# Performance work log

Measured on AMD Instinct MI355X. Metric: run time of the kernel, lower is better.

The kernel has to match this reference:

```python
import jax, jax.numpy as jnp
import numpy as np

B, S, D, H = 2, 2048, 1024, 16
DK = D // H  # 64


def setup_inputs() -> dict:
    key = jax.random.key(0)
    ks = jax.random.split(key, 12)
    inp = {
        "query": jax.random.normal(ks[0], (B, S, D), jnp.float32),
        "key": jax.random.normal(ks[1], (B, S, D), jnp.float32),
        "value": jax.random.normal(ks[2], (B, S, D), jnp.float32),
        "mask": jnp.ones((B, 1, S, S), jnp.float32),  # 1.0 = attend
    }
    sc = 1.0 / np.sqrt(D)
    inp["wq"] = jax.random.normal(ks[3], (D, D), jnp.float32) * sc
    inp["bq"] = jax.random.normal(ks[4], (D,), jnp.float32) * 0.01
    inp["wk"] = jax.random.normal(ks[5], (D, D), jnp.float32) * sc
    inp["bk"] = jax.random.normal(ks[6], (D,), jnp.float32) * 0.01
    inp["wv"] = jax.random.normal(ks[7], (D, D), jnp.float32) * sc
    inp["bv"] = jax.random.normal(ks[8], (D,), jnp.float32) * 0.01
    inp["wo"] = jax.random.normal(ks[9], (D, D), jnp.float32) * sc
    inp["bo"] = jax.random.normal(ks[10], (D,), jnp.float32) * 0.01
    return inp


def _split_heads(x):
    # [B, S, D] -> [B, H, S, DK]
    b, s, _ = x.shape
    return x.reshape(b, s, H, DK).transpose(0, 2, 1, 3)


def reference(query, key, value, mask, wq, bq, wk, bk, wv, bv, wo, bo):
    # Linear projections (torch Linear: x @ W.T + b)
    q = _split_heads(query @ wq.T + bq)   # [B,H,Sq,DK]
    k = _split_heads(key @ wk.T + bk)     # [B,H,Sk,DK]
    v = _split_heads(value @ wv.T + bv)   # [B,H,Sk,DK]

    attn = jnp.einsum('bhqd,bhkd->bhqk', q, k) / jnp.sqrt(jnp.float32(DK))
    # mask: 1.0 attend, 0.0 masked -> add finfo.min at masked positions
    inv = (1.0 - mask) * jnp.finfo(attn.dtype).min
    attn = attn + inv
    attention_weights = jax.nn.softmax(attn, axis=-1)  # [B,H,Sq,Sk]
    # dropout=0.0 (eval mode): identity
    ctx = jnp.einsum('bhqk,bhkd->bhqd', attention_weights, v)  # [B,H,Sq,DK]
    concat = ctx.transpose(0, 2, 1, 3).reshape(ctx.shape[0], ctx.shape[2], D)
    output = concat @ wo.T + bo
    return (output, attention_weights)
```

## Files before the change

kernel.cpp:

```cpp
#include <hip/hip_runtime.h>
#include <cstdint>

typedef short bf16x8 __attribute__((ext_vector_type(8)));
typedef float f32x4 __attribute__((ext_vector_type(4)));

#define NEG_MAX 3.402823466e38f

__device__ __forceinline__ unsigned short f2bf(float f) {
  uint32_t u = __builtin_bit_cast(uint32_t, f);
  u += 0x7FFFu + ((u >> 16) & 1u);
  return (unsigned short)(u >> 16);
}

__device__ __forceinline__ bf16x8 pack8(float4 x, float4 y) {
  bf16x8 r;
  r[0] = (short)f2bf(x.x); r[1] = (short)f2bf(x.y); r[2] = (short)f2bf(x.z); r[3] = (short)f2bf(x.w);
  r[4] = (short)f2bf(y.x); r[5] = (short)f2bf(y.y); r[6] = (short)f2bf(y.z); r[7] = (short)f2bf(y.w);
  return r;
}

__global__ __launch_bounds__(256) void cvt_w(const float* __restrict__ wq, const float* __restrict__ wk,
                                             const float* __restrict__ wv, const float* __restrict__ wo,
                                             unsigned short* __restrict__ out) {
  int i = blockIdx.x * 256 + threadIdx.x;
  const int sel = i >> 18;
  const int idx = i & 0x3FFFF;
  const float* src = (sel == 0) ? wq : (sel == 1) ? wk : (sel == 2) ? wv : wo;
  float4 v = reinterpret_cast<const float4*>(src)[idx];
  ushort4 o;
  o.x = f2bf(v.x); o.y = f2bf(v.y); o.z = f2bf(v.z); o.w = f2bf(v.w);
  reinterpret_cast<ushort4*>(out)[i] = o;
}

__global__ __launch_bounds__(256) void mask_scan(const float* __restrict__ mask,
                                                 int* __restrict__ flags) {
  const int blk = blockIdx.x;
  const int kt = blk & 31, qt = (blk >> 5) & 31, b = blk >> 10;
  const float* base = mask + ((size_t)b * 2048 + qt * 64) * 2048 + kt * 64;
  const int t = threadIdx.x;
  const int row = t >> 2, c0 = (t & 3) * 16;
  const float4* p = reinterpret_cast<const float4*>(base + (size_t)row * 2048 + c0);
  bool ones = true;
#pragma unroll
  for (int i = 0; i < 4; ++i) {
    float4 v = p[i];
    ones = ones && (v.x == 1.f) && (v.y == 1.f) && (v.z == 1.f) && (v.w == 1.f);
  }
  unsigned long long ball = __ballot(ones);
  __shared__ int sf[4];
  if ((t & 63) == 0) sf[t >> 6] = (ball == ~0ull) ? 1 : 0;
  __syncthreads();
  if (t == 0) flags[blk] = sf[0] & sf[1] & sf[2] & sf[3];
}

__global__ __launch_bounds__(256) void gemm_qkv(const float* __restrict__ Aq,
                                                const float* __restrict__ Ak,
                                                const float* __restrict__ Av,
                                                const unsigned short* __restrict__ W3,
                                                const float* __restrict__ bq,
                                                const float* __restrict__ bk,
                                                const float* __restrict__ bv,
                                                unsigned short* __restrict__ Qbf,
                                                unsigned short* __restrict__ Kbf,
                                                unsigned short* __restrict__ Vtb) {
  constexpr int KD = 1024;
  __shared__ __align__(16) unsigned short Al[128 * 32];
  __shared__ __align__(16) unsigned short Bl[128 * 32];
  const int tid = threadIdx.x;
  const int l = tid & 63;
  const int w = tid >> 6;
  const int lr = l & 15;
  const int lg = l >> 4;
  const int gm = blockIdx.y;
  const int gn = blockIdx.x;
  const int z = blockIdx.z;
  const int wr = w >> 1;
  const int wc = w & 1;

  const float* Af = (z == 0) ? Aq : (z == 1) ? Ak : Av;
  const float* bias = (z == 0) ? bq : (z == 1) ? bk : bv;
  const unsigned short* Bw = W3 + (size_t)z * 1048576;
  unsigned short* Cb = (z == 0) ? Qbf : (z == 1) ? Kbf : Vtb;

  f32x4 acc[4][4];
#pragma unroll
  for (int m = 0; m < 4; ++m)
#pragma unroll
    for (int n = 0; n < 4; ++n) acc[m][n] = (f32x4){0.f, 0.f, 0.f, 0.f};

  const int c0 = w * 2;
  const int srow = (l >> 2);
  const int scol = (l & 3) * 8;
  const unsigned short* gB = Bw + (size_t)(gn * 128) * KD;

  const int arow = tid >> 1;
  const int ahalf = tid & 1;
  const float* gA = Af + (size_t)(gm * 128 + arow) * KD + ahalf * 16;

  float4 ap[4];
  {
    const float4* p = reinterpret_cast<const float4*>(gA);
#pragma unroll
    for (int i = 0; i < 4; ++i) ap[i] = p[i];
  }

  for (int kt = 0; kt < 32; ++kt) {
    const int k0 = kt * 32;
    const unsigned short* b0 = gB + (size_t)(c0 * 16 + srow) * KD + k0 + scol;
    const unsigned short* b1 = b0 + (size_t)16 * KD;
    __builtin_amdgcn_global_load_lds((const __attribute__((address_space(1))) void*)b0,
                                     (__attribute__((address_space(3))) void*)&Bl[c0 * 512], 16, 0, 0);
    __builtin_amdgcn_global_load_lds((const __attribute__((address_space(1))) void*)b1,
                                     (__attribute__((address_space(3))) void*)&Bl[c0 * 512 + 512], 16, 0, 0);
    {
      bf16x8* dst = reinterpret_cast<bf16x8*>(&Al[arow * 32 + ahalf * 16]);
      dst[0] = pack8(ap[0], ap[1]);
      dst[1] = pack8(ap[2], ap[3]);
    }
    __syncthreads();
    if (kt + 1 < 32) {
      const float4* p = reinterpret_cast<const float4*>(gA + (kt + 1) * 32);
#pragma unroll
      for (int i = 0; i < 4; ++i) ap[i] = p[i];
    }
    bf16x8 af[4], bfr[4];
#pragma unroll
    for (int m = 0; m < 4; ++m)
      af[m] = *reinterpret_cast<const bf16x8*>(&Al[(wr * 64 + m * 16 + lr) * 32 + lg * 8]);
#pragma unroll
    for (int n = 0; n < 4; ++n)
      bfr[n] = *reinterpret_cast<const bf16x8*>(&Bl[(wc * 64 + n * 16 + lr) * 32 + lg * 8]);
#pragma unroll
    for (int m = 0; m < 4; ++m)
#pragma unroll
      for (int n = 0; n < 4; ++n)
        acc[m][n] = __builtin_amdgcn_mfma_f32_16x16x32_bf16(af[m], bfr[n], acc[m][n], 0, 0, 0);
    __syncthreads();
  }

#pragma unroll
  for (int m = 0; m < 4; ++m) {
#pragma unroll
    for (int n = 0; n < 4; ++n) {
      const int colg = gn * 128 + wc * 64 + n * 16 + lr;
      const float bv2 = bias[colg];
#pragma unroll
      for (int r = 0; r < 4; ++r) {
        const int rowg = gm * 128 + wr * 64 + m * 16 + lg * 4 + r;
        const float v = acc[m][n][r] + bv2;
        const int bb = rowg >> 11, ss = rowg & 2047;
        const int hh = colg >> 6, dk = colg & 63;
        if (z < 2)
          Cb[(((size_t)bb * 16 + hh) * 2048 + ss) * 64 + dk] = f2bf(v);
        else
          Cb[(((size_t)bb * 16 + hh) * 32 + (ss >> 6)) * 4096 + (size_t)dk * 64 + (ss & 63)] = f2bf(v);
      }
    }
  }
}

__global__ __launch_bounds__(256) void gemm_out(const unsigned short* __restrict__ A,
                                                const unsigned short* __restrict__ Bw,
                                                const float* __restrict__ bias,
                                                float* __restrict__ Cf) {
  constexpr int KD = 1024;
  __shared__ __align__(16) unsigned short Al[128 * 32];
  __shared__ __align__(16) unsigned short Bl[128 * 32];
  const int tid = threadIdx.x;
  const int l = tid & 63;
  const int w = tid >> 6;
  const int lr = l & 15;
  const int lg = l >> 4;
  const int gm = blockIdx.y;
  const int gn = blockIdx.x;
  const int wr = w >> 1;
  const int wc = w & 1;

  f32x4 acc[4][4];
#pragma unroll
  for (int m = 0; m < 4; ++m)
#pragma unroll
    for (int n = 0; n < 4; ++n) acc[m][n] = (f32x4){0.f, 0.f, 0.f, 0.f};

  const int c0 = w * 2;
  const int srow = (l >> 2);
  const int scol = (l & 3) * 8;
  const unsigned short* gA = A + (size_t)(gm * 128) * KD;
  const unsigned short* gB = Bw + (size_t)(gn * 128) * KD;

  for (int kt = 0; kt < 32; ++kt) {
    const int k0 = kt * 32;
    const unsigned short* a0 = gA + (size_t)(c0 * 16 + srow) * KD + k0 + scol;
    const unsigned short* a1 = a0 + (size_t)16 * KD;
    const unsigned short* b0 = gB + (size_t)(c0 * 16 + srow) * KD + k0 + scol;
    const unsigned short* b1 = b0 + (size_t)16 * KD;
    __builtin_amdgcn_global_load_lds((const __attribute__((address_space(1))) void*)a0,
                                     (__attribute__((address_space(3))) void*)&Al[c0 * 512], 16, 0, 0);
    __builtin_amdgcn_global_load_lds((const __attribute__((address_space(1))) void*)a1,
                                     (__attribute__((address_space(3))) void*)&Al[c0 * 512 + 512], 16, 0, 0);
    __builtin_amdgcn_global_load_lds((const __attribute__((address_space(1))) void*)b0,
                                     (__attribute__((address_space(3))) void*)&Bl[c0 * 512], 16, 0, 0);
    __builtin_amdgcn_global_load_lds((const __attribute__((address_space(1))) void*)b1,
                                     (__attribute__((address_space(3))) void*)&Bl[c0 * 512 + 512], 16, 0, 0);
    __syncthreads();
    bf16x8 af[4], bfr[4];
#pragma unroll
    for (int m = 0; m < 4; ++m)
      af[m] = *reinterpret_cast<const bf16x8*>(&Al[(wr * 64 + m * 16 + lr) * 32 + lg * 8]);
#pragma unroll
    for (int n = 0; n < 4; ++n)
      bfr[n] = *reinterpret_cast<const bf16x8*>(&Bl[(wc * 64 + n * 16 + lr) * 32 + lg * 8]);
#pragma unroll
    for (int m = 0; m < 4; ++m)
#pragma unroll
      for (int n = 0; n < 4; ++n)
        acc[m][n] = __builtin_amdgcn_mfma_f32_16x16x32_bf16(af[m], bfr[n], acc[m][n], 0, 0, 0);
    __syncthreads();
  }

#pragma unroll
  for (int m = 0; m < 4; ++m) {
#pragma unroll
    for (int n = 0; n < 4; ++n) {
      const int colg = gn * 128 + wc * 64 + n * 16 + lr;
      const float bv = bias[colg];
#pragma unroll
      for (int r = 0; r < 4; ++r) {
        const int rowg = gm * 128 + wr * 64 + m * 16 + lg * 4 + r;
        Cf[(size_t)rowg * 1024 + colg] = acc[m][n][r] + bv;
      }
    }
  }
}

__global__ __launch_bounds__(256, 4) void attn_fused(const unsigned short* __restrict__ Q,
                                                     const unsigned short* __restrict__ Kb,
                                                     const unsigned short* __restrict__ Vt,
                                                     const float* __restrict__ mask,
                                                     const int* __restrict__ flags,
                                                     float* __restrict__ wout,
                                                     unsigned short* __restrict__ ctx) {
  const int tid = threadIdx.x;
  const int l = tid & 63;
  const int w = tid >> 6;
  const int lr = l & 15;
  const int lg = l >> 4;

  const int d = blockIdx.x;
  const int bh = (d >> 8) * 8 + (d & 7);
  const int qt = (d >> 3) & 31;
  const int b = bh >> 4, h = bh & 15;
  const int q0 = qt * 64;

  __shared__ __align__(16) unsigned short KV[4][4096];
  __shared__ __align__(16) unsigned short Wl[4][16][64];

  const size_t qoff = ((size_t)bh * 2048 + (q0 + w * 16 + lr)) * 64 + lg * 8;
  const bf16x8 qf0 = *reinterpret_cast<const bf16x8*>(Q + qoff);
  const bf16x8 qf1 = *reinterpret_cast<const bf16x8*>(Q + qoff + 32);

  const int seg0 = w * 128 + l;
  const int seg1 = seg0 + 64;
  const int r0s = seg0 >> 3, c0x = (seg0 & 7) ^ (r0s & 7);
  const int r1s = seg1 >> 3, c1x = (seg1 & 7) ^ (r1s & 7);
  const unsigned short* kB = Kb + (size_t)bh * 131072;
  const unsigned short* vB = Vt + (size_t)bh * 131072;
  const size_t tS0 = (size_t)r0s * 64 + c0x * 8;
  const size_t tS1 = (size_t)r1s * 64 + c1x * 8;
  const int ldsOff0 = w * 1024;
  const int ldsOff1 = w * 1024 + 512;

  const int sA = (lg ^ (lr & 7)) << 3;
  const int sBo = ((4 + lg) ^ (lr & 7)) << 3;

  const int fbase = (b * 32 + qt) * 32;
  const float* mbase = mask + (size_t)b * 2048 * 2048;

#define STAGE(base_, kt_, slot_)                                                                     \
  do {                                                                                               \
    const unsigned short* s_ = (base_) + (size_t)(kt_) * 4096;                                       \
    unsigned short* d_ = &KV[slot_][0];                                                              \
    __builtin_amdgcn_global_load_lds((const __attribute__((address_space(1))) void*)(s_ + tS0),      \
                                     (__attribute__((address_space(3))) void*)(d_ + ldsOff0), 16, 0, 0); \
    __builtin_amdgcn_global_load_lds((const __attribute__((address_space(1))) void*)(s_ + tS1),      \
                                     (__attribute__((address_space(3))) void*)(d_ + ldsOff1), 16, 0, 0); \
  } while (0)

  float s0[4] = {0.f, 0.f, 0.f, 0.f};

  STAGE(kB, 0, 0);
  STAGE(kB, 1, 1);
  for (int kt = 0; kt < 32; ++kt) {
    if (kt < 31) {
      asm volatile("s_waitcnt vmcnt(2)" ::: "memory");
    } else {
      asm volatile("s_waitcnt vmcnt(0)" ::: "memory");
    }
    __builtin_amdgcn_s_barrier();
    __builtin_amdgcn_sched_barrier(0);
    const unsigned short* Ks = &KV[kt % 3][0];
    bf16x8 kf0[4], kf1[4];
#pragma unroll
    for (int n = 0; n < 4; ++n) {
      const int rb = (n * 16 + lr) * 64;
      kf0[n] = *reinterpret_cast<const bf16x8*>(&Ks[rb + sA]);
      kf1[n] = *reinterpret_cast<const bf16x8*>(&Ks[rb + sBo]);
    }
    if (kt + 2 < 32) STAGE(kB, kt + 2, (kt + 2) % 3);
    f32x4 acc[4];
#pragma unroll
    for (int n = 0; n < 4; ++n) {
      acc[n] = (f32x4){0.f, 0.f, 0.f, 0.f};
      acc[n] = __builtin_amdgcn_mfma_f32_16x16x32_bf16(qf0, kf0[n], acc[n], 0, 0, 0);
      acc[n] = __builtin_amdgcn_mfma_f32_16x16x32_bf16(qf1, kf1[n], acc[n], 0, 0, 0);
    }
    const int fl = flags[fbase + kt];
    if (fl) {
#pragma unroll
      for (int r = 0; r < 4; ++r)
        s0[r] += __expf(acc[0][r] * 0.125f) + __expf(acc[1][r] * 0.125f) +
                 __expf(acc[2][r] * 0.125f) + __expf(acc[3][r] * 0.125f);
    } else {
#pragma unroll
      for (int r = 0; r < 4; ++r) {
        const int qrow = q0 + w * 16 + lg * 4 + r;
        const float* mp = mbase + (size_t)qrow * 2048 + kt * 64;
        float ps = 0.f;
#pragma unroll
        for (int n = 0; n < 4; ++n) {
          const float mv = mp[n * 16 + lr];
          ps += __expf(acc[n][r] * 0.125f + (1.0f - mv) * (-NEG_MAX));
        }
        s0[r] += ps;
      }
    }
  }

  float inv_s[4];
#pragma unroll
  for (int r = 0; r < 4; ++r) {
#pragma unroll
    for (int dd = 1; dd < 16; dd <<= 1) s0[r] += __shfl_xor(s0[r], dd);
    inv_s[r] = 1.0f / s0[r];
  }

  f32x4 cacc[4];
#pragma unroll
  for (int n = 0; n < 4; ++n) cacc[n] = (f32x4){0.f, 0.f, 0.f, 0.f};

  STAGE(kB, 0, 0);
  STAGE(vB, 0, 2);
  for (int kt = 0; kt < 32; ++kt) {
    const int cur = kt & 1;
    asm volatile("s_waitcnt vmcnt(0)" ::: "memory");
    __builtin_amdgcn_s_barrier();
    __builtin_amdgcn_sched_barrier(0);
    const unsigned short* Ks = &KV[cur][0];
    const unsigned short* Vs = &KV[2 + cur][0];
    bf16x8 kf0[4], kf1[4];
#pragma unroll
    for (int n = 0; n < 4; ++n) {
      const int rb = (n * 16 + lr) * 64;
      kf0[n] = *reinterpret_cast<const bf16x8*>(&Ks[rb + sA]);
      kf1[n] = *reinterpret_cast<const bf16x8*>(&Ks[rb + sBo]);
    }
    if (kt + 1 < 32) {
      STAGE(kB, kt + 1, cur ^ 1);
      STAGE(vB, kt + 1, 2 + (cur ^ 1));
    }
    f32x4 acc[4];
#pragma unroll
    for (int n = 0; n < 4; ++n) {
      acc[n] = (f32x4){0.f, 0.f, 0.f, 0.f};
      acc[n] = __builtin_amdgcn_mfma_f32_16x16x32_bf16(qf0, kf0[n], acc[n], 0, 0, 0);
      acc[n] = __builtin_amdgcn_mfma_f32_16x16x32_bf16(qf1, kf1[n], acc[n], 0, 0, 0);
    }
    const int fl = flags[fbase + kt];
#pragma unroll
    for (int r = 0; r < 4; ++r) {
      const int qrow = q0 + w * 16 + lg * 4 + r;
      float* wp = wout + ((size_t)bh * 2048 + qrow) * 2048 + kt * 64;
      const int row2 = lg * 4 + r;
      const int rx = (row2 & 7) << 3;
      if (fl) {
#pragma unroll
        for (int n = 0; n < 4; ++n) {
          const float wgt = __expf(acc[n][r] * 0.125f) * inv_s[r];
          wp[n * 16 + lr] = wgt;
          Wl[w][row2][(n * 16 + lr) ^ rx] = f2bf(wgt);
        }
      } else {
        const float* mp = mbase + (size_t)qrow * 2048 + kt * 64;
#pragma unroll
        for (int n = 0; n < 4; ++n) {
          const float mv = mp[n * 16 + lr];
          const float wgt = __expf(acc[n][r] * 0.125f + (1.0f - mv) * (-NEG_MAX)) * inv_s[r];
          wp[n * 16 + lr] = wgt;
          Wl[w][row2][(n * 16 + lr) ^ rx] = f2bf(wgt);
        }
      }
    }
    bf16x8 vf0[4], vf1[4];
#pragma unroll
    for (int n = 0; n < 4; ++n) {
      const int rb = (n * 16 + lr) * 64;
      vf0[n] = *reinterpret_cast<const bf16x8*>(&Vs[rb + sA]);
      vf1[n] = *reinterpret_cast<const bf16x8*>(&Vs[rb + sBo]);
    }
    asm volatile("s_waitcnt lgkmcnt(0)" ::: "memory");
    __builtin_amdgcn_sched_barrier(0);
    const bf16x8 a0 = *reinterpret_cast<const bf16x8*>(&Wl[w][lr][(lg ^ (lr & 7)) * 8]);
    const bf16x8 a1 = *reinterpret_cast<const bf16x8*>(&Wl[w][lr][((4 | lg) ^ (lr & 7)) * 8]);
#pragma unroll
    for (int n = 0; n < 4; ++n) {
      cacc[n] = __builtin_amdgcn_mfma_f32_16x16x32_bf16(a0, vf0[n], cacc[n], 0, 0, 0);
      cacc[n] = __builtin_amdgcn_mfma_f32_16x16x32_bf16(a1, vf1[n], cacc[n], 0, 0, 0);
    }
  }

#pragma unroll
  for (int n = 0; n < 4; ++n) {
#pragma unroll
    for (int r = 0; r < 4; ++r) {
      const int ss = q0 + w * 16 + lg * 4 + r;
      const int col = h * 64 + n * 16 + lr;
      ctx[((size_t)b * 2048 + ss) * 1024 + col] = f2bf(cacc[n][r]);
    }
  }
#undef STAGE
}

extern "C" void kernel_launch(void* const* d_in, const int* in_sizes, int n_in,
                              void* d_out, int out_size, void* d_ws, size_t ws_size,
                              hipStream_t stream) {
  const float* query = (const float*)d_in[0];
  const float* key   = (const float*)d_in[1];
  const float* value = (const float*)d_in[2];
  const float* mask  = (const float*)d_in[3];
  const float* wq = (const float*)d_in[4];
  const float* bq = (const float*)d_in[5];
  const float* wk = (const float*)d_in[6];
  const float* bk = (const float*)d_in[7];
  const float* wv = (const float*)d_in[8];
  const float* bv = (const float*)d_in[9];
  const float* wo = (const float*)d_in[10];
  const float* bo = (const float*)d_in[11];

  unsigned short* Qbf = (unsigned short*)d_ws;
  unsigned short* Kbf = Qbf + 4194304;
  unsigned short* Vtb = Kbf + 4194304;
  unsigned short* ctx = Vtb + 4194304;
  unsigned short* wbf4 = ctx + 4194304;
  int* flags = (int*)(wbf4 + 4194304);

  float* outp = (float*)d_out;
  float* wout = outp + 4194304;

  mask_scan<<<2048, 256, 0, stream>>>(mask, flags);
  cvt_w<<<4096, 256, 0, stream>>>(wq, wk, wv, wo, wbf4);

  dim3 gq(8, 32, 3);
  gemm_qkv<<<gq, 256, 0, stream>>>(query, key, value, wbf4, bq, bk, bv, Qbf, Kbf, Vtb);

  attn_fused<<<1024, 256, 0, stream>>>(Qbf, Kbf, Vtb, mask, flags, wout, ctx);

  dim3 gg(8, 32);
  gemm_out<<<gg, 256, 0, stream>>>(ctx, wbf4 + 3145728, bo, outp);
}
```

Measured before the change: 311.0 us.

## Widen attention blocks to 128 queries with 8 waves sharing K/V tiles

Each attention block now has 512 threads covering 128 query rows instead of 64. Every K/V tile staged into LDS is therefore reused by twice as many waves, which halves global K/V traffic, and each thread issues a single async load per stage. Per-tile mask flags are loaded once into a ballot bitmask rather than read from global memory every iteration. The attention-weight output is written with nontemporal stores to avoid polluting the cache. The grid is halved to 512 blocks, so there may be fewer blocks per CU and less latency hiding.

```diff
diff --git a/kernel.cpp b/kernel.cpp
--- a/kernel.cpp
+++ b/kernel.cpp
@@ -233,7 +233,7 @@
   }
 }
 
-__global__ __launch_bounds__(256, 4) void attn_fused(const unsigned short* __restrict__ Q,
+__global__ __launch_bounds__(512, 4) void attn_fused(const unsigned short* __restrict__ Q,
                                                      const unsigned short* __restrict__ Kb,
                                                      const unsigned short* __restrict__ Vt,
                                                      const float* __restrict__ mask,
@@ -247,43 +247,38 @@
   const int lg = l >> 4;
 
   const int d = blockIdx.x;
-  const int bh = (d >> 8) * 8 + (d & 7);
-  const int qt = (d >> 3) & 31;
+  const int bh = (d >> 7) * 8 + (d & 7);
+  const int qp = (d >> 3) & 15;
   const int b = bh >> 4, h = bh & 15;
-  const int q0 = qt * 64;
+  const int q0 = qp * 128;
 
   __shared__ __align__(16) unsigned short KV[4][4096];
-  __shared__ __align__(16) unsigned short Wl[4][16][64];
+  __shared__ __align__(16) unsigned short Wl[8][16][64];
 
   const size_t qoff = ((size_t)bh * 2048 + (q0 + w * 16 + lr)) * 64 + lg * 8;
   const bf16x8 qf0 = *reinterpret_cast<const bf16x8*>(Q + qoff);
   const bf16x8 qf1 = *reinterpret_cast<const bf16x8*>(Q + qoff + 32);
 
-  const int seg0 = w * 128 + l;
-  const int seg1 = seg0 + 64;
-  const int r0s = seg0 >> 3, c0x = (seg0 & 7) ^ (r0s & 7);
-  const int r1s = seg1 >> 3, c1x = (seg1 & 7) ^ (r1s & 7);
+  const int seg = tid;
+  const int rs = seg >> 3, cx = (seg & 7) ^ (rs & 7);
   const unsigned short* kB = Kb + (size_t)bh * 131072;
   const unsigned short* vB = Vt + (size_t)bh * 131072;
-  const size_t tS0 = (size_t)r0s * 64 + c0x * 8;
-  const size_t tS1 = (size_t)r1s * 64 + c1x * 8;
-  const int ldsOff0 = w * 1024;
-  const int ldsOff1 = w * 1024 + 512;
+  const size_t tS = (size_t)rs * 64 + cx * 8;
+  const int ldsOff = w * 512;
 
   const int sA = (lg ^ (lr & 7)) << 3;
   const int sBo = ((4 + lg) ^ (lr & 7)) << 3;
 
-  const int fbase = (b * 32 + qt) * 32;
+  const int fbase = (b * 32 + qp * 2 + (w >> 2)) * 32;
+  const uint32_t fmask = (uint32_t)__ballot(flags[fbase + (l & 31)] != 0);
+
   const float* mbase = mask + (size_t)b * 2048 * 2048;
 
-#define STAGE(base_, kt_, slot_)                                                                     \
-  do {                                                                                               \
-    const unsigned short* s_ = (base_) + (size_t)(kt_) * 4096;                                       \
-    unsigned short* d_ = &KV[slot_][0];                                                              \
-    __builtin_amdgcn_global_load_lds((const __attribute__((address_space(1))) void*)(s_ + tS0),      \
-                                     (__attribute__((address_space(3))) void*)(d_ + ldsOff0), 16, 0, 0); \
-    __builtin_amdgcn_global_load_lds((const __attribute__((address_space(1))) void*)(s_ + tS1),      \
-                                     (__attribute__((address_space(3))) void*)(d_ + ldsOff1), 16, 0, 0); \
+#define STAGE(base_, kt_, slot_)                                                                       \
+  do {                                                                                                 \
+    __builtin_amdgcn_global_load_lds(                                                                  \
+        (const __attribute__((address_space(1))) void*)((base_) + (size_t)(kt_) * 4096 + tS),          \
+        (__attribute__((address_space(3))) void*)(&KV[slot_][0] + ldsOff), 16, 0, 0);                  \
   } while (0)
 
   float s0[4] = {0.f, 0.f, 0.f, 0.f};
@@ -292,7 +287,7 @@
   STAGE(kB, 1, 1);
   for (int kt = 0; kt < 32; ++kt) {
     if (kt < 31) {
-      asm volatile("s_waitcnt vmcnt(2)" ::: "memory");
+      asm volatile("s_waitcnt vmcnt(1)" ::: "memory");
     } else {
       asm volatile("s_waitcnt vmcnt(0)" ::: "memory");
     }
@@ -314,8 +309,7 @@
       acc[n] = __builtin_amdgcn_mfma_f32_16x16x32_bf16(qf0, kf0[n], acc[n], 0, 0, 0);
       acc[n] = __builtin_amdgcn_mfma_f32_16x16x32_bf16(qf1, kf1[n], acc[n], 0, 0, 0);
     }
-    const int fl = flags[fbase + kt];
-    if (fl) {
+    if ((fmask >> kt) & 1) {
 #pragma unroll
       for (int r = 0; r < 4; ++r)
         s0[r] += __expf(acc[0][r] * 0.125f) + __expf(acc[1][r] * 0.125f) +
@@ -375,7 +369,7 @@
       acc[n] = __builtin_amdgcn_mfma_f32_16x16x32_bf16(qf0, kf0[n], acc[n], 0, 0, 0);
       acc[n] = __builtin_amdgcn_mfma_f32_16x16x32_bf16(qf1, kf1[n], acc[n], 0, 0, 0);
     }
-    const int fl = flags[fbase + kt];
+    const int fl = (fmask >> kt) & 1;
 #pragma unroll
     for (int r = 0; r < 4; ++r) {
       const int qrow = q0 + w * 16 + lg * 4 + r;
@@ -386,7 +380,7 @@
 #pragma unroll
         for (int n = 0; n < 4; ++n) {
           const float wgt = __expf(acc[n][r] * 0.125f) * inv_s[r];
-          wp[n * 16 + lr] = wgt;
+          __builtin_nontemporal_store(wgt, &wp[n * 16 + lr]);
           Wl[w][row2][(n * 16 + lr) ^ rx] = f2bf(wgt);
         }
       } else {
@@ -395,7 +389,7 @@
         for (int n = 0; n < 4; ++n) {
           const float mv = mp[n * 16 + lr];
           const float wgt = __expf(acc[n][r] * 0.125f + (1.0f - mv) * (-NEG_MAX)) * inv_s[r];
-          wp[n * 16 + lr] = wgt;
+          __builtin_nontemporal_store(wgt, &wp[n * 16 + lr]);
           Wl[w][row2][(n * 16 + lr) ^ rx] = f2bf(wgt);
         }
       }
@@ -462,7 +456,7 @@
   dim3 gq(8, 32, 3);
   gemm_qkv<<<gq, 256, 0, stream>>>(query, key, value, wbf4, bq, bk, bv, Qbf, Kbf, Vtb);
 
-  attn_fused<<<1024, 256, 0, stream>>>(Qbf, Kbf, Vtb, mask, flags, wout, ctx);
+  attn_fused<<<512, 512, 0, stream>>>(Qbf, Kbf, Vtb, mask, flags, wout, ctx);
 
   dim3 gg(8, 32);
   gemm_out<<<gg, 256, 0, stream>>>(ctx, wbf4 + 3145728, bo, outp);
```

Measured after the change: 309.2 us. Within noise of the previous version (-0.6%).
